# Optimization experiments

Hardware: AMD Instinct MI355X
Metric: run time of the kernel (lower is better)

Reference implementation:

```python
import jax, jax.numpy as jnp
import numpy as np

REG = 0.1  # config['reg']


def _poly_filter(s, gammas):
    # Horner evaluation of sum_k gammas[k] * s**k (monomial basis, depth K=len-1).
    out = jnp.full_like(s, gammas[-1])
    for k in range(gammas.shape[0] - 2, -1, -1):
        out = out * s + gammas[k]
    return out


def setup_inputs() -> dict:
    key = jax.random.key(0)
    k1, k2, k3, k4, k5 = jax.random.split(key, 5)
    B, H, N, R = 4, 8, 4096, 64
    U = jax.random.normal(k1, (B, H, N, R), dtype=jnp.float32)
    Sigma = jax.random.normal(k2, (B, H, 1, R), dtype=jnp.float32)
    svd_V = jax.random.normal(k3, (B, H, N, R), dtype=jnp.float32)
    V = jax.random.normal(k4, (B, H, N, R), dtype=jnp.float32)
    mask = jnp.ones((B, N), dtype=jnp.float32)
    # learnable polynomial coefficients; gamma_0 fixed to 1 (fixI=True)
    gammas = jnp.concatenate([jnp.ones((1,), jnp.float32),
                              0.1 * jax.random.normal(k5, (4,), dtype=jnp.float32)])
    return {"U": U, "Sigma": Sigma, "svd_V": svd_V, "V": V, "mask": mask, "gammas": gammas}


def reference(U, Sigma, svd_V, V, mask, gammas):
    # Q: softmax over rank dim r
    Q = jax.nn.softmax(U, axis=-1)                                      # [B,H,N,r]
    # K: masked softmax over sequence dim N
    Kmat = jax.nn.softmax(svd_V - 1e9 * (1.0 - mask[:, None, :, None]), axis=-2)
    S = jax.nn.sigmoid(Sigma)                                           # [B,H,1,r]
    graph_filter = _poly_filter(S, gammas)                              # [B,H,1,r]
    # linear-attention ordering: (Q*filt) @ (K^T @ V), never forms NxN
    KtV = jnp.einsum('bhnr,bhnd->bhrd', Kmat, V)                        # [B,H,r,d]
    X = jnp.einsum('bhnr,bhrd->bhnd', Q * graph_filter, KtV)            # [B,H,N,d]
    r = Q.shape[-1]
    eye = jnp.eye(r, dtype=Q.dtype)
    symQ = jnp.einsum('bhnr,bhns->bhrs', Q, Q) - eye
    ortho_loss = REG * jnp.mean(jnp.abs(symQ), axis=(1, 2, 3))
    symK = jnp.einsum('bhnr,bhns->bhrs', Kmat, Kmat) - eye
    ortho_loss = ortho_loss + REG * jnp.mean(jnp.abs(symK), axis=(1, 2, 3))
    return X, ortho_loss
```

## Files before the change

kernel.cpp:

```cpp
#include <hip/hip_runtime.h>
#include <math.h>

#define NB 4
#define NH 8
#define BHN 32
#define SN 4096
#define RR 64
#define REGC 0.1f

#define MCH 16
#define MROWS 256
#define XCH 32
#define XROWS 128

typedef short s16x8 __attribute__((ext_vector_type(8)));
typedef float f32x4 __attribute__((ext_vector_type(4)));

__device__ __forceinline__ float wave_sum(float v) {
    #pragma unroll
    for (int off = 32; off; off >>= 1) v += __shfl_xor(v, off, 64);
    return v;
}
__device__ __forceinline__ float wave_sum64(float v) {
    v += __int_as_float(__builtin_amdgcn_update_dpp(0, __float_as_int(v), 0x121, 0xf, 0xf, true));
    v += __int_as_float(__builtin_amdgcn_update_dpp(0, __float_as_int(v), 0x122, 0xf, 0xf, true));
    v += __int_as_float(__builtin_amdgcn_update_dpp(0, __float_as_int(v), 0x124, 0xf, 0xf, true));
    v += __int_as_float(__builtin_amdgcn_update_dpp(0, __float_as_int(v), 0x128, 0xf, 0xf, true));
    v += __shfl_xor(v, 16, 64);
    v += __shfl_xor(v, 32, 64);
    return v;
}
__device__ __forceinline__ float octet_sum(float v) {
    v += __int_as_float(__builtin_amdgcn_update_dpp(0, __float_as_int(v), 0xB1, 0xf, 0xf, true));
    v += __int_as_float(__builtin_amdgcn_update_dpp(0, __float_as_int(v), 0x4E, 0xf, 0xf, true));
    v += __shfl_xor(v, 4, 64);
    return v;
}
__device__ __forceinline__ unsigned short f2bf(float x) {
    unsigned int u = __float_as_uint(x);
    u += 0x7FFFu + ((u >> 16) & 1u);
    return (unsigned short)(u >> 16);
}
__device__ __forceinline__ float bf2f(unsigned short h) {
    return __uint_as_float(((unsigned int)h) << 16);
}
__device__ __forceinline__ unsigned int packbf(float a, float b) {
    return (unsigned int)f2bf(a) | ((unsigned int)f2bf(b) << 16);
}
__device__ __forceinline__ s16x8 ldfrag(const unsigned int* p) {
    uint4 r = *(const uint4*)p;
    return __builtin_bit_cast(s16x8, r);
}
__device__ __forceinline__ int swz(int row, int blk) {
    return (row << 5) + (((blk ^ (row & 7))) << 2);
}
__device__ __forceinline__ uint4 pack8(const float* x) {
    return make_uint4(packbf(x[0], x[1]), packbf(x[2], x[3]),
                      packbf(x[4], x[5]), packbf(x[6], x[7]));
}

__global__ void k_zero_loss(float* loss) {
    if (threadIdx.x < NB) loss[threadIdx.x] = 0.0f;
}

#define PH 0
#define VH 2048
#define QH 4096
__launch_bounds__(512, 4)
__global__ void k_main(const float* __restrict__ U, const float* __restrict__ sv,
                       const float* __restrict__ V, const float* __restrict__ mask,
                       float* __restrict__ ktv_part, float* __restrict__ symk_part,
                       float* __restrict__ symq_part, float* __restrict__ colsum_part) {
    __shared__ __align__(16) unsigned int sm[12288];
    const int chunk = blockIdx.x, bh = blockIdx.y, b = bh >> 3;
    const int t = threadIdx.x, l = t & 63, w = t >> 6;
    const int r15 = l & 15, quad = l >> 4;
    const int ni = w & 3, mi0 = (w >> 2) << 1;
    const size_t rowbase = (size_t)bh * SN * RR;
    const int row0 = chunk * MROWS;

    float csum = 0.0f;
    f32x4 aKV[2], aSK[2], aSQ[2];
    #pragma unroll
    for (int j = 0; j < 2; j++) {
        aKV[j] = (f32x4){0.f, 0.f, 0.f, 0.f};
        aSK[j] = (f32x4){0.f, 0.f, 0.f, 0.f};
        aSQ[j] = (f32x4){0.f, 0.f, 0.f, 0.f};
    }

    float bu[2][8], bx[2][8], bv[2][8];
    #pragma unroll
    for (int i = 0; i < 8; i++) {
        const size_t off = rowbase + (size_t)(row0 + 8 * w + i) * RR + l;
        bu[0][i] = U[off]; bx[0][i] = sv[off]; bv[0][i] = V[off];
    }

    #pragma unroll
    for (int s = 0; s < 4; s++) {
        const int cur = s & 1, nxt = cur ^ 1;
        const int nb = row0 + s * 64;
        const int bufb = cur * 6144;
        float bm[8];
        #pragma unroll
        for (int i = 0; i < 8; i++) bm[i] = mask[b * SN + nb + 8 * w + i];
        float q[8], p[8];
        #pragma unroll
        for (int i = 0; i < 8; i++) {
            const float eu = __expf(bu[cur][i]);
            q[i] = eu * (1.0f / wave_sum64(eu));
        }
        #pragma unroll
        for (int i = 0; i < 8; i++) {
            p[i] = __expf(bx[cur][i] - 1e9f * (1.0f - bm[i]));
            csum += p[i];
        }
        if (s < 3) {
            #pragma unroll
            for (int i = 0; i < 8; i++) {
                const size_t off = rowbase + (size_t)(nb + 64 + 8 * w + i) * RR + l;
                bu[nxt][i] = U[off]; bx[nxt][i] = sv[off]; bv[nxt][i] = V[off];
            }
        }
        const uint4 ph = pack8(p);
        const uint4 vh = pack8(bv[cur]);
        const uint4 qh = pack8(q);
        const int wbase = bufb + (l << 5) + ((w ^ (l & 7)) << 2);
        *(uint4*)(sm + PH + wbase) = ph;
        *(uint4*)(sm + VH + wbase) = vh;
        *(uint4*)(sm + QH + wbase) = qh;
        __syncthreads();
        #pragma unroll
        for (int ks = 0; ks < 2; ks++) {
            const int ub = ks * 4 + quad;
            s16x8 Ah[2], AQ[2];
            #pragma unroll
            for (int j = 0; j < 2; j++) {
                const int oa = bufb + swz((mi0 + j) * 16 + r15, ub);
                Ah[j] = ldfrag(sm + PH + oa);
                AQ[j] = ldfrag(sm + QH + oa);
            }
            const int ob = bufb + swz(ni * 16 + r15, ub);
            const s16x8 Bvh = ldfrag(sm + VH + ob);
            const s16x8 Bph = ldfrag(sm + PH + ob);
            const s16x8 Bq  = ldfrag(sm + QH + ob);
            #pragma unroll
            for (int j = 0; j < 2; j++) {
                aKV[j] = __builtin_amdgcn_mfma_f32_16x16x32_bf16(Ah[j], Bvh, aKV[j], 0, 0, 0);
                aSK[j] = __builtin_amdgcn_mfma_f32_16x16x32_bf16(Ah[j], Bph, aSK[j], 0, 0, 0);
                aSQ[j] = __builtin_amdgcn_mfma_f32_16x16x32_bf16(AQ[j], Bq,  aSQ[j], 0, 0, 0);
            }
        }
    }
    const size_t pb = ((size_t)bh * MCH + chunk) * 4096;
    #pragma unroll
    for (int j = 0; j < 2; j++)
        #pragma unroll
        for (int r = 0; r < 4; r++) {
            const int e = ((mi0 + j) * 16 + quad * 4 + r) * 64 + ni * 16 + r15;
            ktv_part[pb + e]  = aKV[j][r];
            symk_part[pb + e] = aSK[j][r];
            symq_part[pb + e] = aSQ[j][r];
        }
    __syncthreads();
    float* smf = (float*)sm;
    smf[w * 64 + l] = csum;
    __syncthreads();
    if (w == 0) {
        float scol = 0.f;
        #pragma unroll
        for (int j = 0; j < 8; j++) scol += smf[j * 64 + l];
        colsum_part[(bh * MCH + chunk) * 64 + l] = scol;
    }
}

__global__ void k_finalize(const float* __restrict__ ktv_part, const float* __restrict__ symk_part,
                           const float* __restrict__ symq_part, const float* __restrict__ colsum_part,
                           const float* __restrict__ Sigma, const float* __restrict__ gammas,
                           unsigned short* __restrict__ ktvt_hi, unsigned short* __restrict__ ktvt_lo,
                           float* __restrict__ loss) {
    const int rb = blockIdx.x, bh = blockIdx.y, b = bh >> 3, t = threadIdx.x;
    __shared__ float cs[64];
    if (t < 64) {
        float s = 0.f;
        for (int c = 0; c < MCH; c++) s += colsum_part[(bh * MCH + c) * 64 + t];
        cs[t] = s;
    }
    __syncthreads();
    const float g0 = gammas[0], g1 = gammas[1], g2 = gammas[2], g3 = gammas[3], g4 = gammas[4];
    float lsum = 0.0f;
    #pragma unroll
    for (int o = 0; o < 2; o++) {
        const int idx = rb * 512 + o * 256 + t;
        const int r = idx >> 6, c = idx & 63;
        float kv = 0.f, sk = 0.f, sq = 0.f;
        for (int ch = 0; ch < MCH; ch++) {
            const size_t pb = ((size_t)bh * MCH + ch) * 4096 + idx;
            kv += ktv_part[pb]; sk += symk_part[pb]; sq += symq_part[pb];
        }
        const float iSr = 1.0f / cs[r], iSc = 1.0f / cs[c];
        kv *= iSr;
        sk *= iSr * iSc;
        const float sg = 1.0f / (1.0f + __expf(-Sigma[bh * 64 + r]));
        float f = g4; f = f * sg + g3; f = f * sg + g2; f = f * sg + g1; f = f * sg + g0;
        const float kvf = kv * f;
        const unsigned short h = f2bf(kvf);
        ktvt_hi[bh * 4096 + c * 64 + r] = h;
        ktvt_lo[bh * 4096 + c * 64 + r] = f2bf(kvf - bf2f(h));
        const float eye = (r == c) ? 1.0f : 0.0f;
        lsum += fabsf(sk - eye) + fabsf(sq - eye);
    }
    lsum = wave_sum(lsum);
    __shared__ float smr[4];
    if ((t & 63) == 0) smr[t >> 6] = lsum;
    __syncthreads();
    if (t == 0)
        atomicAdd(loss + b, (REGC / (NH * 64.0f * 64.0f)) * (smr[0] + smr[1] + smr[2] + smr[3]));
}

__launch_bounds__(512, 8)
__global__ void k_xq(const float* __restrict__ U,
                     const unsigned short* __restrict__ ktvt_hi,
                     const unsigned short* __restrict__ ktvt_lo,
                     float* __restrict__ Xout) {
    __shared__ __align__(16) unsigned int sm[4096];
    const int chunk = blockIdx.x, bh = blockIdx.y;
    const int t = threadIdx.x, l = t & 63, w = t >> 6;
    const int r15 = l & 15, quad = l >> 4;
    const int ni = w & 3, mi0 = (w >> 2) << 1;
    const size_t rowbase = (size_t)bh * SN * RR;
    const int row0 = chunk * XROWS;
    const int nl = 8 * w + (l >> 3);
    const int c0 = (l & 7) * 8;

    s16x8 Bh[2], Bl[2];
    #pragma unroll
    for (int ks = 0; ks < 2; ks++) {
        const int idx = (ni * 16 + r15) * 64 + ks * 32 + quad * 8;
        Bh[ks] = __builtin_bit_cast(s16x8, *(const uint4*)(ktvt_hi + (size_t)bh * 4096 + idx));
        Bl[ks] = __builtin_bit_cast(s16x8, *(const uint4*)(ktvt_lo + (size_t)bh * 4096 + idx));
    }

    float4 ba[2], bb[2];
    {
        const float* src = U + rowbase + (size_t)(row0 + nl) * RR + c0;
        ba[0] = *(const float4*)src;
        bb[0] = *(const float4*)(src + 4);
    }

    #pragma unroll
    for (int s = 0; s < 2; s++) {
        const int cur = s & 1, nxt = cur ^ 1;
        const int nb = row0 + s * 64;
        const int bufb = cur * 2048;
        float e[8];
        e[0] = __expf(ba[cur].x); e[1] = __expf(ba[cur].y);
        e[2] = __expf(ba[cur].z); e[3] = __expf(ba[cur].w);
        e[4] = __expf(bb[cur].x); e[5] = __expf(bb[cur].y);
        e[6] = __expf(bb[cur].z); e[7] = __expf(bb[cur].w);
        float loc = 0.f;
        #pragma unroll
        for (int i = 0; i < 8; i++) loc += e[i];
        const float inv = 1.0f / octet_sum(loc);
        if (s < 1) {
            const float* src = U + rowbase + (size_t)(nb + 64 + nl) * RR + c0;
            ba[nxt] = *(const float4*)src;
            bb[nxt] = *(const float4*)(src + 4);
        }
        float q[8];
        #pragma unroll
        for (int i = 0; i < 8; i++) q[i] = e[i] * inv;
        *(uint4*)(sm + bufb + swz(nl, l & 7)) = pack8(q);
        __syncthreads();
        f32x4 acc[2];
        acc[0] = (f32x4){0.f, 0.f, 0.f, 0.f};
        acc[1] = (f32x4){0.f, 0.f, 0.f, 0.f};
        #pragma unroll
        for (int ks = 0; ks < 2; ks++) {
            #pragma unroll
            for (int jj = 0; jj < 2; jj++) {
                const int oa = bufb + swz((mi0 + jj) * 16 + r15, ks * 4 + quad);
                const s16x8 Ah = ldfrag(sm + oa);
                acc[jj] = __builtin_amdgcn_mfma_f32_16x16x32_bf16(Ah, Bh[ks], acc[jj], 0, 0, 0);
                acc[jj] = __builtin_amdgcn_mfma_f32_16x16x32_bf16(Ah, Bl[ks], acc[jj], 0, 0, 0);
            }
        }
        #pragma unroll
        for (int jj = 0; jj < 2; jj++)
            #pragma unroll
            for (int r = 0; r < 4; r++) {
                const int n = nb + (mi0 + jj) * 16 + quad * 4 + r;
                Xout[rowbase + (size_t)n * RR + ni * 16 + r15] = acc[jj][r];
            }
    }
}

extern "C" void kernel_launch(void* const* d_in, const int* in_sizes, int n_in,
                              void* d_out, int out_size, void* d_ws, size_t ws_size,
                              hipStream_t stream) {
    (void)in_sizes; (void)n_in; (void)out_size; (void)ws_size;
    const float* U      = (const float*)d_in[0];
    const float* Sigma  = (const float*)d_in[1];
    const float* sv     = (const float*)d_in[2];
    const float* V      = (const float*)d_in[3];
    const float* mask   = (const float*)d_in[4];
    const float* gammas = (const float*)d_in[5];

    float* X    = (float*)d_out;
    float* loss = X + (size_t)BHN * SN * RR;

    float* ws          = (float*)d_ws;
    float* ktv_part    = ws;
    float* symk_part   = ktv_part + (size_t)BHN * MCH * 4096;
    float* symq_part   = symk_part + (size_t)BHN * MCH * 4096;
    float* colsum_part = symq_part + (size_t)BHN * MCH * 4096;
    unsigned short* ktvt_hi = (unsigned short*)(colsum_part + BHN * MCH * 64);
    unsigned short* ktvt_lo = ktvt_hi + BHN * 4096;

    hipLaunchKernelGGL(k_zero_loss, dim3(1), dim3(64), 0, stream, loss);
    hipLaunchKernelGGL(k_main, dim3(MCH, BHN), dim3(512), 0, stream,
                       U, sv, V, mask, ktv_part, symk_part, symq_part, colsum_part);
    hipLaunchKernelGGL(k_finalize, dim3(8, BHN), dim3(256), 0, stream,
                       ktv_part, symk_part, symq_part, colsum_part, Sigma, gammas,
                       ktvt_hi, ktvt_lo, loss);
    hipLaunchKernelGGL(k_xq, dim3(XCH, BHN), dim3(512), 0, stream,
                       U, ktvt_hi, ktvt_lo, X);
}
```

Before: 157.7 us.

## Reduce per-chunk partials with global atomics and move loss reduction into k_xq

k_main now accumulates KtV, symK, symQ and column sums straight into per-head workspace buffers with float atomicAdd, replacing per-chunk partial arrays that k_finalize had to sum. This removes the partial-buffer write/read traffic and the serial 16-way reduction loop in k_finalize. A zeroing kernel clears the accumulators, and the loss is written from per-block partials inside k_xq instead of via atomics. Prefetches of the next tile are issued earlier, and divisions use raw v_rcp_f32. The trade-offs are atomic contention, nondeterministic summation order, and slightly less accurate reciprocals.

```diff
diff --git a/kernel.cpp b/kernel.cpp
--- a/kernel.cpp
+++ b/kernel.cpp
@@ -36,6 +36,9 @@
     v += __shfl_xor(v, 4, 64);
     return v;
 }
+__device__ __forceinline__ float fastrcp(float x) {
+    float r; asm("v_rcp_f32 %0, %1" : "=v"(r) : "v"(x)); return r;
+}
 __device__ __forceinline__ unsigned short f2bf(float x) {
     unsigned int u = __float_as_uint(x);
     u += 0x7FFFu + ((u >> 16) & 1u);
@@ -59,8 +62,10 @@
                       packbf(x[4], x[5]), packbf(x[6], x[7]));
 }
 
-__global__ void k_zero_loss(float* loss) {
-    if (threadIdx.x < NB) loss[threadIdx.x] = 0.0f;
+#define ZF4 98880
+__global__ void k_zero_ws(float4* ws) {
+    const int i = blockIdx.x * 256 + threadIdx.x;
+    if (i < ZF4) ws[i] = make_float4(0.f, 0.f, 0.f, 0.f);
 }
 
 #define PH 0
@@ -69,8 +74,8 @@
 __launch_bounds__(512, 4)
 __global__ void k_main(const float* __restrict__ U, const float* __restrict__ sv,
                        const float* __restrict__ V, const float* __restrict__ mask,
-                       float* __restrict__ ktv_part, float* __restrict__ symk_part,
-                       float* __restrict__ symq_part, float* __restrict__ colsum_part) {
+                       float* __restrict__ ktv_acc, float* __restrict__ symk_acc,
+                       float* __restrict__ symq_acc, float* __restrict__ colsum_acc) {
     __shared__ __align__(16) unsigned int sm[12288];
     const int chunk = blockIdx.x, bh = blockIdx.y, b = bh >> 3;
     const int t = threadIdx.x, l = t & 63, w = t >> 6;
@@ -100,6 +105,13 @@
         const int cur = s & 1, nxt = cur ^ 1;
         const int nb = row0 + s * 64;
         const int bufb = cur * 6144;
+        if (s < 3) {
+            #pragma unroll
+            for (int i = 0; i < 8; i++) {
+                const size_t off = rowbase + (size_t)(nb + 64 + 8 * w + i) * RR + l;
+                bu[nxt][i] = U[off]; bx[nxt][i] = sv[off]; bv[nxt][i] = V[off];
+            }
+        }
         float bm[8];
         #pragma unroll
         for (int i = 0; i < 8; i++) bm[i] = mask[b * SN + nb + 8 * w + i];
@@ -107,19 +119,12 @@
         #pragma unroll
         for (int i = 0; i < 8; i++) {
             const float eu = __expf(bu[cur][i]);
-            q[i] = eu * (1.0f / wave_sum64(eu));
+            q[i] = eu * fastrcp(wave_sum64(eu));
         }
         #pragma unroll
         for (int i = 0; i < 8; i++) {
             p[i] = __expf(bx[cur][i] - 1e9f * (1.0f - bm[i]));
             csum += p[i];
-        }
-        if (s < 3) {
-            #pragma unroll
-            for (int i = 0; i < 8; i++) {
-                const size_t off = rowbase + (size_t)(nb + 64 + 8 * w + i) * RR + l;
-                bu[nxt][i] = U[off]; bx[nxt][i] = sv[off]; bv[nxt][i] = V[off];
-            }
         }
         const uint4 ph = pack8(p);
         const uint4 vh = pack8(bv[cur]);
@@ -151,40 +156,27 @@
             }
         }
     }
-    const size_t pb = ((size_t)bh * MCH + chunk) * 4096;
+    const size_t ab = (size_t)bh * 4096;
     #pragma unroll
     for (int j = 0; j < 2; j++)
         #pragma unroll
         for (int r = 0; r < 4; r++) {
             const int e = ((mi0 + j) * 16 + quad * 4 + r) * 64 + ni * 16 + r15;
-            ktv_part[pb + e]  = aKV[j][r];
-            symk_part[pb + e] = aSK[j][r];
-            symq_part[pb + e] = aSQ[j][r];
-        }
-    __syncthreads();
-    float* smf = (float*)sm;
-    smf[w * 64 + l] = csum;
-    __syncthreads();
-    if (w == 0) {
-        float scol = 0.f;
-        #pragma unroll
-        for (int j = 0; j < 8; j++) scol += smf[j * 64 + l];
-        colsum_part[(bh * MCH + chunk) * 64 + l] = scol;
-    }
-}
-
-__global__ void k_finalize(const float* __restrict__ ktv_part, const float* __restrict__ symk_part,
-                           const float* __restrict__ symq_part, const float* __restrict__ colsum_part,
+            atomicAdd(ktv_acc + ab + e,  aKV[j][r]);
+            atomicAdd(symk_acc + ab + e, aSK[j][r]);
+            atomicAdd(symq_acc + ab + e, aSQ[j][r]);
+        }
+    atomicAdd(colsum_acc + bh * 64 + l, csum);
+}
+
+__global__ void k_finalize(const float* __restrict__ ktv_acc, const float* __restrict__ symk_acc,
+                           const float* __restrict__ symq_acc, const float* __restrict__ colsum_acc,
                            const float* __restrict__ Sigma, const float* __restrict__ gammas,
                            unsigned short* __restrict__ ktvt_hi, unsigned short* __restrict__ ktvt_lo,
-                           float* __restrict__ loss) {
-    const int rb = blockIdx.x, bh = blockIdx.y, b = bh >> 3, t = threadIdx.x;
+                           float* __restrict__ loss_part) {
+    const int rb = blockIdx.x, bh = blockIdx.y, t = threadIdx.x;
     __shared__ float cs[64];
-    if (t < 64) {
-        float s = 0.f;
-        for (int c = 0; c < MCH; c++) s += colsum_part[(bh * MCH + c) * 64 + t];
-        cs[t] = s;
-    }
+    if (t < 64) cs[t] = colsum_acc[bh * 64 + t];
     __syncthreads();
     const float g0 = gammas[0], g1 = gammas[1], g2 = gammas[2], g3 = gammas[3], g4 = gammas[4];
     float lsum = 0.0f;
@@ -192,15 +184,12 @@
     for (int o = 0; o < 2; o++) {
         const int idx = rb * 512 + o * 256 + t;
         const int r = idx >> 6, c = idx & 63;
-        float kv = 0.f, sk = 0.f, sq = 0.f;
-        for (int ch = 0; ch < MCH; ch++) {
-            const size_t pb = ((size_t)bh * MCH + ch) * 4096 + idx;
-            kv += ktv_part[pb]; sk += symk_part[pb]; sq += symq_part[pb];
-        }
-        const float iSr = 1.0f / cs[r], iSc = 1.0f / cs[c];
+        const size_t pb = (size_t)bh * 4096 + idx;
+        float kv = ktv_acc[pb], sk = symk_acc[pb], sq = symq_acc[pb];
+        const float iSr = fastrcp(cs[r]), iSc = fastrcp(cs[c]);
         kv *= iSr;
         sk *= iSr * iSc;
-        const float sg = 1.0f / (1.0f + __expf(-Sigma[bh * 64 + r]));
+        const float sg = fastrcp(1.0f + __expf(-Sigma[bh * 64 + r]));
         float f = g4; f = f * sg + g3; f = f * sg + g2; f = f * sg + g1; f = f * sg + g0;
         const float kvf = kv * f;
         const unsigned short h = f2bf(kvf);
@@ -213,15 +202,15 @@
     __shared__ float smr[4];
     if ((t & 63) == 0) smr[t >> 6] = lsum;
     __syncthreads();
-    if (t == 0)
-        atomicAdd(loss + b, (REGC / (NH * 64.0f * 64.0f)) * (smr[0] + smr[1] + smr[2] + smr[3]));
+    if (t == 0) loss_part[bh * 8 + rb] = smr[0] + smr[1] + smr[2] + smr[3];
 }
 
 __launch_bounds__(512, 8)
 __global__ void k_xq(const float* __restrict__ U,
                      const unsigned short* __restrict__ ktvt_hi,
                      const unsigned short* __restrict__ ktvt_lo,
-                     float* __restrict__ Xout) {
+                     const float* __restrict__ loss_part,
+                     float* __restrict__ Xout, float* __restrict__ loss) {
     __shared__ __align__(16) unsigned int sm[4096];
     const int chunk = blockIdx.x, bh = blockIdx.y;
     const int t = threadIdx.x, l = t & 63, w = t >> 6;
@@ -232,6 +221,11 @@
     const int nl = 8 * w + (l >> 3);
     const int c0 = (l & 7) * 8;
 
+    if (chunk == 0 && bh == 0 && t < 256) {
+        const float v = wave_sum(loss_part[t]);
+        if ((t & 63) == 0) loss[t >> 6] = (REGC / (NH * 64.0f * 64.0f)) * v;
+    }
+
     s16x8 Bh[2], Bl[2];
     #pragma unroll
     for (int ks = 0; ks < 2; ks++) {
@@ -252,6 +246,11 @@
         const int cur = s & 1, nxt = cur ^ 1;
         const int nb = row0 + s * 64;
         const int bufb = cur * 2048;
+        if (s < 1) {
+            const float* src = U + rowbase + (size_t)(nb + 64 + nl) * RR + c0;
+            ba[nxt] = *(const float4*)src;
+            bb[nxt] = *(const float4*)(src + 4);
+        }
         float e[8];
         e[0] = __expf(ba[cur].x); e[1] = __expf(ba[cur].y);
         e[2] = __expf(ba[cur].z); e[3] = __expf(ba[cur].w);
@@ -260,12 +259,7 @@
         float loc = 0.f;
         #pragma unroll
         for (int i = 0; i < 8; i++) loc += e[i];
-        const float inv = 1.0f / octet_sum(loc);
-        if (s < 1) {
-            const float* src = U + rowbase + (size_t)(nb + 64 + nl) * RR + c0;
-            ba[nxt] = *(const float4*)src;
-            bb[nxt] = *(const float4*)(src + 4);
-        }
+        const float inv = fastrcp(octet_sum(loc));
         float q[8];
         #pragma unroll
         for (int i = 0; i < 8; i++) q[i] = e[i] * inv;
@@ -309,19 +303,20 @@
     float* loss = X + (size_t)BHN * SN * RR;
 
     float* ws          = (float*)d_ws;
-    float* ktv_part    = ws;
-    float* symk_part   = ktv_part + (size_t)BHN * MCH * 4096;
-    float* symq_part   = symk_part + (size_t)BHN * MCH * 4096;
-    float* colsum_part = symq_part + (size_t)BHN * MCH * 4096;
-    unsigned short* ktvt_hi = (unsigned short*)(colsum_part + BHN * MCH * 64);
+    float* ktv_acc     = ws;
+    float* symk_acc    = ktv_acc + (size_t)BHN * 4096;
+    float* symq_acc    = symk_acc + (size_t)BHN * 4096;
+    float* colsum_acc  = symq_acc + (size_t)BHN * 4096;
+    float* loss_part   = colsum_acc + BHN * 64;
+    unsigned short* ktvt_hi = (unsigned short*)(loss_part + 256);
     unsigned short* ktvt_lo = ktvt_hi + BHN * 4096;
 
-    hipLaunchKernelGGL(k_zero_loss, dim3(1), dim3(64), 0, stream, loss);
+    hipLaunchKernelGGL(k_zero_ws, dim3((ZF4 + 255) / 256), dim3(256), 0, stream, (float4*)ws);
     hipLaunchKernelGGL(k_main, dim3(MCH, BHN), dim3(512), 0, stream,
-                       U, sv, V, mask, ktv_part, symk_part, symq_part, colsum_part);
+                       U, sv, V, mask, ktv_acc, symk_acc, symq_acc, colsum_acc);
     hipLaunchKernelGGL(k_finalize, dim3(8, BHN), dim3(256), 0, stream,
-                       ktv_part, symk_part, symq_part, colsum_part, Sigma, gammas,
-                       ktvt_hi, ktvt_lo, loss);
+                       ktv_acc, symk_acc, symq_acc, colsum_acc, Sigma, gammas,
+                       ktvt_hi, ktvt_lo, loss_part);
     hipLaunchKernelGGL(k_xq, dim3(XCH, BHN), dim3(512), 0, stream,
-                       U, ktvt_hi, ktvt_lo, X);
-}
+                       U, ktvt_hi, ktvt_lo, loss_part, X, loss);
+}
```

Measured after the change: 171.4 us. +8.7%, slower.
